# Kernel tuning notes

Hardware: AMD Instinct MI355X
Metric: run time of the kernel (lower is better)

The kernel has to match this reference:

```python
import jax, jax.numpy as jnp
import numpy as np

B, Q, K, DQ, DK, DV, H = 16, 64, 512, 512, 512, 512, 256
MASK_VAL = -1e6


def setup_inputs() -> dict:
    key = jax.random.key(0)
    k1, k2, k3, k4, k5, k6, k7 = jax.random.split(key, 7)
    return {
        "queries": jax.random.normal(k1, (B, Q, DQ), dtype=jnp.float32),
        "keys": jax.random.normal(k2, (B, K, DK), dtype=jnp.float32),
        "values": jax.random.normal(k3, (B, K, DV), dtype=jnp.float32),
        "valid_lens": jax.random.randint(k4, (B,), 1, K + 1, dtype=jnp.int32),
        "Wq": jax.random.normal(k5, (DQ, H), dtype=jnp.float32) * (1.0 / np.sqrt(DQ)),
        "Wk": jax.random.normal(k6, (DK, H), dtype=jnp.float32) * (1.0 / np.sqrt(DK)),
        "Wv": jax.random.normal(k7, (H,), dtype=jnp.float32) * (1.0 / np.sqrt(H)),
    }


def reference(queries, keys, values, valid_lens, Wq, Wk, Wv):
    # Project queries and keys into the shared additive-attention space.
    q = jnp.einsum("bqd,dh->bqh", queries, Wq)   # [B,Q,H]
    k = jnp.einsum("bkd,dh->bkh", keys, Wk)      # [B,K,H]
    # Bahdanau additive scoring: tanh(q + k) projected to a scalar per (q,k).
    feats = jnp.tanh(q[:, :, None, :] + k[:, None, :, :])  # [B,Q,K,H]
    scores = jnp.einsum("bqkh,h->bqk", feats, Wv)           # [B,Q,K]
    # Masked softmax over the key axis (positions >= valid_len masked out).
    mask = jnp.arange(K)[None, None, :] < valid_lens[:, None, None]  # [B,1,K]
    scores = jnp.where(mask, scores, MASK_VAL)
    attn = jax.nn.softmax(scores, axis=-1)                  # [B,Q,K]
    # Dropout is identity in eval mode; weighted sum of values.
    return jnp.einsum("bqk,bkv->bqv", attn, values)         # [B,Q,DV]
```

## Files before the change

kernel.cpp:

```cpp
#include <hip/hip_runtime.h>

#define LOG2E 1.4426950408889634f
#define TWO_LOG2E 2.8853900817779268f

typedef __attribute__((ext_vector_type(8))) short short8;
typedef __attribute__((ext_vector_type(4))) float f32x4;

__device__ __forceinline__ float e2x(float v) {
    return __builtin_amdgcn_exp2f(v * TWO_LOG2E);
}

__device__ __forceinline__ void split2(float x, float y, unsigned& hi, unsigned& lo) {
    unsigned ux = __float_as_uint(x), uy = __float_as_uint(y);
    float hx = __uint_as_float(ux & 0xffff0000u);
    float hy = __uint_as_float(uy & 0xffff0000u);
    unsigned lx = __float_as_uint(x - hx), ly = __float_as_uint(y - hy);
    hi = (ux >> 16) | (uy & 0xffff0000u);
    lo = (lx >> 16) | (ly & 0xffff0000u);
}

__global__ __launch_bounds__(256) void wprep_kernel(const float* __restrict__ Wq,
                                                    const float* __restrict__ Wk,
                                                    ushort* __restrict__ Wq2T,
                                                    ushort* __restrict__ Wk2T) {
    __shared__ float T[64][65];
    const float* W  = blockIdx.z ? Wk : Wq;
    ushort* W2T     = blockIdx.z ? Wk2T : Wq2T;
    const int t  = threadIdx.x;
    const int k0 = blockIdx.x * 64;
    const int n0 = blockIdx.y * 64;
#pragma unroll
    for (int p = 0; p < 4; ++p) {
        int u  = t + p * 256;
        int kk = u >> 4;
        int nf = (u & 15) * 4;
        float4 w = *reinterpret_cast<const float4*>(&W[(size_t)(k0 + kk) * 256 + n0 + nf]);
        T[nf + 0][kk] = w.x; T[nf + 1][kk] = w.y;
        T[nf + 2][kk] = w.z; T[nf + 3][kk] = w.w;
    }
    __syncthreads();
#pragma unroll
    for (int p = 0; p < 4; ++p) {
        int u  = t + p * 256;
        int n  = u >> 4;
        int kf = (u & 15) * 4;
        float a = T[n][kf], b = T[n][kf + 1], c = T[n][kf + 2], d = T[n][kf + 3];
        unsigned h01, l01, h23, l23;
        split2(a, b, h01, l01);
        split2(c, d, h23, l23);
        int kg = k0 + kf;
        ushort* row = W2T + (size_t)(n0 + n) * 1536 + (kg >> 5) * 96 + (kg & 31);
        uint2 hi; hi.x = h01; hi.y = h23;
        uint2 lo; lo.x = l01; lo.y = l23;
        *reinterpret_cast<uint2*>(row)      = hi;
        *reinterpret_cast<uint2*>(row + 32) = hi;
        *reinterpret_cast<uint2*>(row + 64) = lo;
    }
}

__global__ __launch_bounds__(256) void mfma_proj_kernel(const float* __restrict__ queries,
                                                        const float* __restrict__ keys,
                                                        const ushort* __restrict__ Wq2T,
                                                        const ushort* __restrict__ Wk2T,
                                                        float* __restrict__ Eq,
                                                        float* __restrict__ Ekp) {
    __shared__ float smemf[7680];
    ushort* Ah = reinterpret_cast<ushort*>(smemf);
    ushort* Ws = reinterpret_cast<ushort*>(smemf) + 3072;

    const int t    = threadIdx.x;
    const int mt   = blockIdx.x;
    const int Nb   = blockIdx.y * 128;
    const bool isQ = mt < 32;
    const int mloc = (isQ ? mt : mt - 32) * 32;
    const float4* Asrc4 = reinterpret_cast<const float4*>(isQ ? queries : keys)
                        + (size_t)mloc * 128;
    const ushort* W2T = isQ ? Wq2T : Wk2T;

    const int ln15 = t & 15;
    const int q    = (t >> 4) & 3;
    const int w    = t >> 6;
    const int wn   = w * 32;
    const int am   = t >> 3;
    const int ak   = t & 7;

    const char* gB[6];
#pragma unroll
    for (int i = 0; i < 6; ++i) {
        int o   = i * 4096 + t * 16;
        int row = o / 192;
        int rem = o - row * 192;
        gB[i] = reinterpret_cast<const char*>(W2T) + (size_t)(Nb + row) * 3072 + rem;
    }

    f32x4 acc[2][2];
#pragma unroll
    for (int fm = 0; fm < 2; ++fm)
#pragma unroll
        for (int fn = 0; fn < 2; ++fn) acc[fm][fn] = (f32x4)0.0f;

    float4 ra = Asrc4[(size_t)am * 128 + ak];

    for (int c = 0; c < 16; ++c) {
        __syncthreads();
#pragma unroll
        for (int i = 0; i < 6; ++i) {
            __builtin_amdgcn_global_load_lds(
                reinterpret_cast<const unsigned int*>(gB[i]),
                reinterpret_cast<unsigned int*>(
                    reinterpret_cast<char*>(Ah) + 6144 + i * 4096 + (t >> 6) * 1024),
                16, 0, 0);
            gB[i] += 192;
        }
        {
            unsigned h01, l01, h23, l23;
            split2(ra.x, ra.y, h01, l01);
            split2(ra.z, ra.w, h23, l23);
            uint2 hi; hi.x = h01; hi.y = h23;
            uint2 lo; lo.x = l01; lo.y = l23;
            ushort* row = Ah + am * 96 + ak * 4;
            *reinterpret_cast<uint2*>(row)      = hi;
            *reinterpret_cast<uint2*>(row + 32) = lo;
            *reinterpret_cast<uint2*>(row + 64) = hi;
        }
        if (c < 15) ra = Asrc4[(size_t)am * 128 + (c + 1) * 8 + ak];
        __syncthreads();
#pragma unroll
        for (int s = 0; s < 3; ++s) {
            short8 af[2], bf[2];
#pragma unroll
            for (int fm = 0; fm < 2; ++fm)
                af[fm] = *reinterpret_cast<const short8*>(
                    Ah + (fm * 16 + ln15) * 96 + s * 32 + q * 8);
#pragma unroll
            for (int fn = 0; fn < 2; ++fn)
                bf[fn] = *reinterpret_cast<const short8*>(
                    Ws + (wn + fn * 16 + ln15) * 96 + s * 32 + q * 8);
#pragma unroll
            for (int fm = 0; fm < 2; ++fm)
#pragma unroll
                for (int fn = 0; fn < 2; ++fn)
                    acc[fm][fn] = __builtin_amdgcn_mfma_f32_16x16x32_bf16(
                        af[fm], bf[fn], acc[fm][fn], 0, 0, 0);
        }
    }

    if (isQ) {
#pragma unroll
        for (int fm = 0; fm < 2; ++fm)
#pragma unroll
            for (int fn = 0; fn < 2; ++fn)
#pragma unroll
                for (int r = 0; r < 4; ++r) {
                    int row = mloc + fm * 16 + q * 4 + r;
                    int col = Nb + wn + fn * 16 + ln15;
                    Eq[(size_t)row * 256 + col] = e2x(acc[fm][fn][r]);
                }
    } else {
        __syncthreads();
        float (*Cs)[33] = reinterpret_cast<float(*)[33]>(smemf);
#pragma unroll
        for (int fm = 0; fm < 2; ++fm)
#pragma unroll
            for (int fn = 0; fn < 2; ++fn)
#pragma unroll
                for (int r = 0; r < 4; ++r) {
                    int m_l = fm * 16 + q * 4 + r;
                    int n_l = wn + fn * 16 + ln15;
                    Cs[n_l][m_l] = acc[fm][fn][r];
                }
        __syncthreads();
        const int b      = mloc >> 9;
        const int k0h    = (mloc & 511) >> 1;
        const int h2base = Nb >> 1;
        float4* out4 = reinterpret_cast<float4*>(Ekp);
#pragma unroll
        for (int p = 0; p < 4; ++p) {
            int u   = t + p * 256;
            int h2r = u >> 4;
            int kp  = u & 15;
            int kk  = kp * 2;
            float4 o;
            o.x = e2x(Cs[2 * h2r    ][kk    ]);
            o.y = e2x(Cs[2 * h2r + 1][kk    ]);
            o.z = e2x(Cs[2 * h2r    ][kk + 1]);
            o.w = e2x(Cs[2 * h2r + 1][kk + 1]);
            out4[(size_t)b * 32768 + (size_t)(h2base + h2r) * 256 + k0h + kp] = o;
        }
    }
}

__global__ __launch_bounds__(256) void score_softmax_kernel(
        const float* __restrict__ Eq, const float* __restrict__ Ekp,
        const float* __restrict__ Wv, const int* __restrict__ valid_lens,
        float* __restrict__ attn) {
    __shared__ float redmA[4], redmB[4], redlA[4], redlB[4];

    const int t  = threadIdx.x;
    const int bq = blockIdx.x;
    const int b  = bq >> 5;
    const int q0 = (bq & 31) * 2;

    const float* eqA = Eq + (size_t)(b * 64 + q0) * 256;
    const float* eqB = eqA + 256;
    const float4* ek4 = reinterpret_cast<const float4*>(Ekp) + (size_t)b * 32768 + t;

    float accA0 = 0.f, accA1 = 0.f, accB0 = 0.f, accB1 = 0.f;
#pragma unroll 4
    for (int h2 = 0; h2 < 128; ++h2) {
        const float4 ek = ek4[h2 * 256];
        const float w0 = Wv[2 * h2];
        const float w1 = Wv[2 * h2 + 1];
        {
            const float e0 = eqA[2 * h2], e1 = eqA[2 * h2 + 1];
            float a00 = fmaf(e0, ek.x, 1.0f);
            float a10 = fmaf(e1, ek.y, 1.0f);
            float a01 = fmaf(e0, ek.z, 1.0f);
            float a11 = fmaf(e1, ek.w, 1.0f);
            float d0 = a00 * a10, d1 = a01 * a11;
            float n0 = fmaf(w1, a00, w0 * a10);
            float n1 = fmaf(w1, a01, w0 * a11);
            accA0 = fmaf(n0, __builtin_amdgcn_rcpf(d0), accA0);
            accA1 = fmaf(n1, __builtin_amdgcn_rcpf(d1), accA1);
        }
        {
            const float e0 = eqB[2 * h2], e1 = eqB[2 * h2 + 1];
            float a00 = fmaf(e0, ek.x, 1.0f);
            float a10 = fmaf(e1, ek.y, 1.0f);
            float a01 = fmaf(e0, ek.z, 1.0f);
            float a11 = fmaf(e1, ek.w, 1.0f);
            float d0 = a00 * a10, d1 = a01 * a11;
            float n0 = fmaf(w1, a00, w0 * a10);
            float n1 = fmaf(w1, a01, w0 * a11);
            accB0 = fmaf(n0, __builtin_amdgcn_rcpf(d0), accB0);
            accB1 = fmaf(n1, __builtin_amdgcn_rcpf(d1), accB1);
        }
    }
    float sA0 = -2.0f * accA0, sA1 = -2.0f * accA1;
    float sB0 = -2.0f * accB0, sB1 = -2.0f * accB1;
    const int vl = valid_lens[b];
    const int k0 = 2 * t;
    if (k0     >= vl) { sA0 = -1e6f; sB0 = -1e6f; }
    if (k0 + 1 >= vl) { sA1 = -1e6f; sB1 = -1e6f; }

    const int w = t >> 6;
    float mA = fmaxf(sA0, sA1);
    float mB = fmaxf(sB0, sB1);
#pragma unroll
    for (int off = 32; off > 0; off >>= 1) {
        mA = fmaxf(mA, __shfl_xor(mA, off));
        mB = fmaxf(mB, __shfl_xor(mB, off));
    }
    if ((t & 63) == 0) { redmA[w] = mA; redmB[w] = mB; }
    __syncthreads();
    mA = fmaxf(fmaxf(redmA[0], redmA[1]), fmaxf(redmA[2], redmA[3]));
    mB = fmaxf(fmaxf(redmB[0], redmB[1]), fmaxf(redmB[2], redmB[3]));

    float pA0 = __builtin_amdgcn_exp2f((sA0 - mA) * LOG2E);
    float pA1 = __builtin_amdgcn_exp2f((sA1 - mA) * LOG2E);
    float pB0 = __builtin_amdgcn_exp2f((sB0 - mB) * LOG2E);
    float pB1 = __builtin_amdgcn_exp2f((sB1 - mB) * LOG2E);
    float lA = pA0 + pA1, lB = pB0 + pB1;
#pragma unroll
    for (int off = 32; off > 0; off >>= 1) {
        lA += __shfl_xor(lA, off);
        lB += __shfl_xor(lB, off);
    }
    if ((t & 63) == 0) { redlA[w] = lA; redlB[w] = lB; }
    __syncthreads();
    lA = (redlA[0] + redlA[1]) + (redlA[2] + redlA[3]);
    lB = (redlB[0] + redlB[1]) + (redlB[2] + redlB[3]);
    const float invA = 1.0f / lA;
    const float invB = 1.0f / lB;

    float2* attn2 = reinterpret_cast<float2*>(attn);
    float2 oA; oA.x = pA0 * invA; oA.y = pA1 * invA;
    float2 oB; oB.x = pB0 * invB; oB.y = pB1 * invB;
    attn2[(size_t)(b * 64 + q0) * 256 + t]       = oA;
    attn2[(size_t)(b * 64 + q0 + 1) * 256 + t]   = oB;
}

__global__ __launch_bounds__(256) void pv_kernel(const float* __restrict__ attn,
                                                 const float* __restrict__ values,
                                                 float* __restrict__ out) {
    __shared__ __align__(16) float Ps[8][516];
    __shared__ __align__(16) float Vs[2][32][128];

    const int t  = threadIdx.x;
    const int b  = blockIdx.z;
    const int q0 = blockIdx.y * 8;
    const int vt = blockIdx.x;

    const float4* attn4 = reinterpret_cast<const float4*>(attn) + (size_t)(b * 64 + q0) * 128;
#pragma unroll
    for (int p = 0; p < 4; ++p) {
        int u  = t + p * 256;
        int qr = u >> 7;
        int c4 = u & 127;
        *reinterpret_cast<float4*>(&Ps[qr][c4 * 4]) = attn4[(size_t)qr * 128 + c4];
    }

    const char* vbase = reinterpret_cast<const char*>(values)
                      + ((size_t)b * 512 * 512 + (size_t)vt * 128) * 4
                      + (size_t)(t >> 5) * 2048 + (size_t)(t & 31) * 16;
    char* ldsV0 = reinterpret_cast<char*>(&Vs[0][0][0]) + (t >> 6) * 1024;

    const int lane = t & 63;
    const int w    = t >> 6;
    const int v4   = lane & 31;
    const int ksub = lane >> 5;

    float4 acc0 = make_float4(0.f, 0.f, 0.f, 0.f);
    float4 acc1 = make_float4(0.f, 0.f, 0.f, 0.f);

#pragma unroll
    for (int i = 0; i < 4; ++i)
        __builtin_amdgcn_global_load_lds(
            reinterpret_cast<const unsigned int*>(vbase + (size_t)i * 8 * 2048),
            reinterpret_cast<unsigned int*>(ldsV0 + i * 4096), 16, 0, 0);
    __syncthreads();

    for (int c = 0; c < 16; ++c) {
        if (c < 15) {
            char* dst = reinterpret_cast<char*>(&Vs[(c + 1) & 1][0][0]) + (t >> 6) * 1024;
            const char* src = vbase + (size_t)(c + 1) * 65536;
#pragma unroll
            for (int i = 0; i < 4; ++i)
                __builtin_amdgcn_global_load_lds(
                    reinterpret_cast<const unsigned int*>(src + (size_t)i * 8 * 2048),
                    reinterpret_cast<unsigned int*>(dst + i * 4096), 16, 0, 0);
        }

        const float (*V)[128] = Vs[c & 1];
        const float* pr0 = &Ps[2 * w][c * 32];
        const float* pr1 = &Ps[2 * w + 1][c * 32];
#pragma unroll
        for (int kk = 0; kk < 4; ++kk) {
            int kb = kk * 8 + ksub * 4;
            float4 V0 = *reinterpret_cast<const float4*>(&V[kb + 0][v4 * 4]);
            float4 V1 = *reinterpret_cast<const float4*>(&V[kb + 1][v4 * 4]);
            float4 V2 = *reinterpret_cast<const float4*>(&V[kb + 2][v4 * 4]);
            float4 V3 = *reinterpret_cast<const float4*>(&V[kb + 3][v4 * 4]);
            float4 p0 = *reinterpret_cast<const float4*>(&pr0[kb]);
            float4 p1 = *reinterpret_cast<const float4*>(&pr1[kb]);
            acc0.x = fmaf(p0.x, V0.x, acc0.x); acc0.y = fmaf(p0.x, V0.y, acc0.y);
            acc0.z = fmaf(p0.x, V0.z, acc0.z); acc0.w = fmaf(p0.x, V0.w, acc0.w);
            acc0.x = fmaf(p0.y, V1.x, acc0.x); acc0.y = fmaf(p0.y, V1.y, acc0.y);
            acc0.z = fmaf(p0.y, V1.z, acc0.z); acc0.w = fmaf(p0.y, V1.w, acc0.w);
            acc0.x = fmaf(p0.z, V2.x, acc0.x); acc0.y = fmaf(p0.z, V2.y, acc0.y);
            acc0.z = fmaf(p0.z, V2.z, acc0.z); acc0.w = fmaf(p0.z, V2.w, acc0.w);
            acc0.x = fmaf(p0.w, V3.x, acc0.x); acc0.y = fmaf(p0.w, V3.y, acc0.y);
            acc0.z = fmaf(p0.w, V3.z, acc0.z); acc0.w = fmaf(p0.w, V3.w, acc0.w);
            acc1.x = fmaf(p1.x, V0.x, acc1.x); acc1.y = fmaf(p1.x, V0.y, acc1.y);
            acc1.z = fmaf(p1.x, V0.z, acc1.z); acc1.w = fmaf(p1.x, V0.w, acc1.w);
            acc1.x = fmaf(p1.y, V1.x, acc1.x); acc1.y = fmaf(p1.y, V1.y, acc1.y);
            acc1.z = fmaf(p1.y, V1.z, acc1.z); acc1.w = fmaf(p1.y, V1.w, acc1.w);
            acc1.x = fmaf(p1.z, V2.x, acc1.x); acc1.y = fmaf(p1.z, V2.y, acc1.y);
            acc1.z = fmaf(p1.z, V2.z, acc1.z); acc1.w = fmaf(p1.z, V2.w, acc1.w);
            acc1.x = fmaf(p1.w, V3.x, acc1.x); acc1.y = fmaf(p1.w, V3.y, acc1.y);
            acc1.z = fmaf(p1.w, V3.z, acc1.z); acc1.w = fmaf(p1.w, V3.w, acc1.w);
        }
        __syncthreads();
    }

    acc0.x += __shfl_xor(acc0.x, 32); acc0.y += __shfl_xor(acc0.y, 32);
    acc0.z += __shfl_xor(acc0.z, 32); acc0.w += __shfl_xor(acc0.w, 32);
    acc1.x += __shfl_xor(acc1.x, 32); acc1.y += __shfl_xor(acc1.y, 32);
    acc1.z += __shfl_xor(acc1.z, 32); acc1.w += __shfl_xor(acc1.w, 32);
    if (ksub == 0) {
        float4* out4 = reinterpret_cast<float4*>(out);
        out4[(size_t)(b * 64 + q0 + 2 * w) * 128 + vt * 32 + v4]     = acc0;
        out4[(size_t)(b * 64 + q0 + 2 * w + 1) * 128 + vt * 32 + v4] = acc1;
    }
}

extern "C" void kernel_launch(void* const* d_in, const int* in_sizes, int n_in,
                              void* d_out, int out_size, void* d_ws, size_t ws_size,
                              hipStream_t stream) {
    (void)in_sizes; (void)n_in; (void)out_size; (void)ws_size;
    const float* queries    = (const float*)d_in[0];
    const float* keys       = (const float*)d_in[1];
    const float* values     = (const float*)d_in[2];
    const int*   valid_lens = (const int*)d_in[3];
    const float* Wq         = (const float*)d_in[4];
    const float* Wk         = (const float*)d_in[5];
    const float* Wv         = (const float*)d_in[6];
    float* out = (float*)d_out;

    float* ws    = (float*)d_ws;
    float* Eq    = ws;
    float* Ekp   = ws + 262144;
    float* attn  = ws + 262144 + 2097152;
    ushort* Wq2T = (ushort*)(ws + 2883584);
    ushort* Wk2T = Wq2T + 393216;

    hipLaunchKernelGGL(wprep_kernel, dim3(8, 4, 2), dim3(256), 0, stream,
                       Wq, Wk, Wq2T, Wk2T);
    hipLaunchKernelGGL(mfma_proj_kernel, dim3(288, 2), dim3(256), 0, stream,
                       queries, keys, Wq2T, Wk2T, Eq, Ekp);
    hipLaunchKernelGGL(score_softmax_kernel, dim3(512), dim3(256), 0, stream,
                       Eq, Ekp, Wv, valid_lens, attn);
    hipLaunchKernelGGL(pv_kernel, dim3(4, 8, 16), dim3(256), 0, stream, attn, values, out);
}
```

Measured before the change: 141.6 us.

## Retile score kernel over 8 queries and move softmax into PV kernel

The score kernel now processes 8 queries by 128 keys per block, staging Eq and Wv in shared memory and splitting the H dimension across two thread halves, so each Ek load is reused across 8 queries instead of 2. It writes raw masked scores. The softmax max, exp and normalisation move into the PV kernel, which computes them on the score rows already staged in LDS, removing block-wide reductions from the score kernel. The cost is redundant softmax work, since each of the 4 value-tile blocks recomputes the softmax for the same rows, plus an extra LDS partial-sum pass in the score kernel.

```diff
diff --git a/kernel.cpp b/kernel.cpp
--- a/kernel.cpp
+++ b/kernel.cpp
@@ -190,97 +190,64 @@
     }
 }
 
-__global__ __launch_bounds__(256) void score_softmax_kernel(
+__global__ __launch_bounds__(256) void score_raw_kernel(
         const float* __restrict__ Eq, const float* __restrict__ Ekp,
         const float* __restrict__ Wv, const int* __restrict__ valid_lens,
-        float* __restrict__ attn) {
-    __shared__ float redmA[4], redmB[4], redlA[4], redlB[4];
-
+        float* __restrict__ scores) {
+    __shared__ float Eqs[8][256];
+    __shared__ float Wvs[256];
+    __shared__ float Sh[2][8][128];
     const int t  = threadIdx.x;
-    const int bq = blockIdx.x;
-    const int b  = bq >> 5;
-    const int q0 = (bq & 31) * 2;
-
-    const float* eqA = Eq + (size_t)(b * 64 + q0) * 256;
-    const float* eqB = eqA + 256;
-    const float4* ek4 = reinterpret_cast<const float4*>(Ekp) + (size_t)b * 32768 + t;
-
-    float accA0 = 0.f, accA1 = 0.f, accB0 = 0.f, accB1 = 0.f;
+    const int kb = blockIdx.x * 128;
+    const int q0 = blockIdx.y * 8;
+    const int b  = blockIdx.z;
+
+    const float4* eq4 = reinterpret_cast<const float4*>(Eq + (size_t)(b * 64 + q0) * 256);
+#pragma unroll
+    for (int i = 0; i < 2; ++i) {
+        int u = t + i * 256;
+        *reinterpret_cast<float4*>(&Eqs[u >> 6][(u & 63) * 4]) = eq4[u];
+    }
+    Wvs[t] = Wv[t];
+    __syncthreads();
+
+    const int kl = t & 127;
+    const int hh = t >> 7;
+    const float2* ek2 = reinterpret_cast<const float2*>(Ekp)
+                      + (size_t)b * 65536 + (size_t)hh * 32768 + kb + kl;
+
+    float acc[8] = {0.f, 0.f, 0.f, 0.f, 0.f, 0.f, 0.f, 0.f};
 #pragma unroll 4
-    for (int h2 = 0; h2 < 128; ++h2) {
-        const float4 ek = ek4[h2 * 256];
-        const float w0 = Wv[2 * h2];
-        const float w1 = Wv[2 * h2 + 1];
-        {
-            const float e0 = eqA[2 * h2], e1 = eqA[2 * h2 + 1];
-            float a00 = fmaf(e0, ek.x, 1.0f);
-            float a10 = fmaf(e1, ek.y, 1.0f);
-            float a01 = fmaf(e0, ek.z, 1.0f);
-            float a11 = fmaf(e1, ek.w, 1.0f);
-            float d0 = a00 * a10, d1 = a01 * a11;
-            float n0 = fmaf(w1, a00, w0 * a10);
-            float n1 = fmaf(w1, a01, w0 * a11);
-            accA0 = fmaf(n0, __builtin_amdgcn_rcpf(d0), accA0);
-            accA1 = fmaf(n1, __builtin_amdgcn_rcpf(d1), accA1);
-        }
-        {
-            const float e0 = eqB[2 * h2], e1 = eqB[2 * h2 + 1];
-            float a00 = fmaf(e0, ek.x, 1.0f);
-            float a10 = fmaf(e1, ek.y, 1.0f);
-            float a01 = fmaf(e0, ek.z, 1.0f);
-            float a11 = fmaf(e1, ek.w, 1.0f);
-            float d0 = a00 * a10, d1 = a01 * a11;
-            float n0 = fmaf(w1, a00, w0 * a10);
-            float n1 = fmaf(w1, a01, w0 * a11);
-            accB0 = fmaf(n0, __builtin_amdgcn_rcpf(d0), accB0);
-            accB1 = fmaf(n1, __builtin_amdgcn_rcpf(d1), accB1);
-        }
-    }
-    float sA0 = -2.0f * accA0, sA1 = -2.0f * accA1;
-    float sB0 = -2.0f * accB0, sB1 = -2.0f * accB1;
+    for (int i = 0; i < 64; ++i) {
+        float2 ek = ek2[(size_t)i * 512];
+        int h2 = hh * 64 + i;
+        float w0 = Wvs[2 * h2], w1 = Wvs[2 * h2 + 1];
+#pragma unroll
+        for (int q = 0; q < 8; ++q) {
+            float e0 = Eqs[q][2 * h2], e1 = Eqs[q][2 * h2 + 1];
+            float a0 = fmaf(e0, ek.x, 1.0f);
+            float a1 = fmaf(e1, ek.y, 1.0f);
+            float d  = a0 * a1;
+            float n  = fmaf(w1, a0, w0 * a1);
+            acc[q] = fmaf(n, __builtin_amdgcn_rcpf(d), acc[q]);
+        }
+    }
+#pragma unroll
+    for (int q = 0; q < 8; ++q) Sh[hh][q][kl] = acc[q];
+    __syncthreads();
+
     const int vl = valid_lens[b];
-    const int k0 = 2 * t;
-    if (k0     >= vl) { sA0 = -1e6f; sB0 = -1e6f; }
-    if (k0 + 1 >= vl) { sA1 = -1e6f; sB1 = -1e6f; }
-
-    const int w = t >> 6;
-    float mA = fmaxf(sA0, sA1);
-    float mB = fmaxf(sB0, sB1);
-#pragma unroll
-    for (int off = 32; off > 0; off >>= 1) {
-        mA = fmaxf(mA, __shfl_xor(mA, off));
-        mB = fmaxf(mB, __shfl_xor(mB, off));
-    }
-    if ((t & 63) == 0) { redmA[w] = mA; redmB[w] = mB; }
-    __syncthreads();
-    mA = fmaxf(fmaxf(redmA[0], redmA[1]), fmaxf(redmA[2], redmA[3]));
-    mB = fmaxf(fmaxf(redmB[0], redmB[1]), fmaxf(redmB[2], redmB[3]));
-
-    float pA0 = __builtin_amdgcn_exp2f((sA0 - mA) * LOG2E);
-    float pA1 = __builtin_amdgcn_exp2f((sA1 - mA) * LOG2E);
-    float pB0 = __builtin_amdgcn_exp2f((sB0 - mB) * LOG2E);
-    float pB1 = __builtin_amdgcn_exp2f((sB1 - mB) * LOG2E);
-    float lA = pA0 + pA1, lB = pB0 + pB1;
-#pragma unroll
-    for (int off = 32; off > 0; off >>= 1) {
-        lA += __shfl_xor(lA, off);
-        lB += __shfl_xor(lB, off);
-    }
-    if ((t & 63) == 0) { redlA[w] = lA; redlB[w] = lB; }
-    __syncthreads();
-    lA = (redlA[0] + redlA[1]) + (redlA[2] + redlA[3]);
-    lB = (redlB[0] + redlB[1]) + (redlB[2] + redlB[3]);
-    const float invA = 1.0f / lA;
-    const float invB = 1.0f / lB;
-
-    float2* attn2 = reinterpret_cast<float2*>(attn);
-    float2 oA; oA.x = pA0 * invA; oA.y = pA1 * invA;
-    float2 oB; oB.x = pB0 * invB; oB.y = pB1 * invB;
-    attn2[(size_t)(b * 64 + q0) * 256 + t]       = oA;
-    attn2[(size_t)(b * 64 + q0 + 1) * 256 + t]   = oB;
-}
-
-__global__ __launch_bounds__(256) void pv_kernel(const float* __restrict__ attn,
+#pragma unroll
+    for (int i = 0; i < 4; ++i) {
+        int u = t + i * 256;
+        int q = u >> 7, k = u & 127;
+        float s = -2.0f * (Sh[0][q][k] + Sh[1][q][k]);
+        if (kb + k >= vl) s = -1e6f;
+        scores[(size_t)(b * 64 + q0 + q) * 512 + kb + k] = s;
+    }
+}
+
+__global__ __launch_bounds__(256) void pv_kernel(const float* __restrict__ scores,
                                                  const float* __restrict__ values,
                                                  float* __restrict__ out) {
     __shared__ __align__(16) float Ps[8][516];
@@ -291,13 +258,13 @@
     const int q0 = blockIdx.y * 8;
     const int vt = blockIdx.x;
 
-    const float4* attn4 = reinterpret_cast<const float4*>(attn) + (size_t)(b * 64 + q0) * 128;
+    const float4* sc4 = reinterpret_cast<const float4*>(scores) + (size_t)(b * 64 + q0) * 128;
 #pragma unroll
     for (int p = 0; p < 4; ++p) {
         int u  = t + p * 256;
         int qr = u >> 7;
         int c4 = u & 127;
-        *reinterpret_cast<float4*>(&Ps[qr][c4 * 4]) = attn4[(size_t)qr * 128 + c4];
+        *reinterpret_cast<float4*>(&Ps[qr][c4 * 4]) = sc4[(size_t)qr * 128 + c4];
     }
 
     const char* vbase = reinterpret_cast<const char*>(values)
@@ -309,9 +276,6 @@
     const int w    = t >> 6;
     const int v4   = lane & 31;
     const int ksub = lane >> 5;
-
-    float4 acc0 = make_float4(0.f, 0.f, 0.f, 0.f);
-    float4 acc1 = make_float4(0.f, 0.f, 0.f, 0.f);
 
 #pragma unroll
     for (int i = 0; i < 4; ++i)
@@ -319,6 +283,31 @@
             reinterpret_cast<const unsigned int*>(vbase + (size_t)i * 8 * 2048),
             reinterpret_cast<unsigned int*>(ldsV0 + i * 4096), 16, 0, 0);
     __syncthreads();
+
+#pragma unroll
+    for (int rr = 0; rr < 2; ++rr) {
+        const int r = 2 * w + rr;
+        float v[8];
+        float m = -1e30f;
+#pragma unroll
+        for (int i = 0; i < 8; ++i) { v[i] = Ps[r][lane + i * 64]; m = fmaxf(m, v[i]); }
+#pragma unroll
+        for (int off = 32; off > 0; off >>= 1) m = fmaxf(m, __shfl_xor(m, off));
+        float s = 0.f;
+#pragma unroll
+        for (int i = 0; i < 8; ++i) {
+            v[i] = __builtin_amdgcn_exp2f((v[i] - m) * LOG2E);
+            s += v[i];
+        }
+#pragma unroll
+        for (int off = 32; off > 0; off >>= 1) s += __shfl_xor(s, off);
+        float inv = 1.0f / s;
+#pragma unroll
+        for (int i = 0; i < 8; ++i) Ps[r][lane + i * 64] = v[i] * inv;
+    }
+
+    float4 acc0 = make_float4(0.f, 0.f, 0.f, 0.f);
+    float4 acc1 = make_float4(0.f, 0.f, 0.f, 0.f);
 
     for (int c = 0; c < 16; ++c) {
         if (c < 15) {
@@ -387,18 +376,19 @@
     const float* Wv         = (const float*)d_in[6];
     float* out = (float*)d_out;
 
-    float* ws    = (float*)d_ws;
-    float* Eq    = ws;
-    float* Ekp   = ws + 262144;
-    float* attn  = ws + 262144 + 2097152;
-    ushort* Wq2T = (ushort*)(ws + 2883584);
-    ushort* Wk2T = Wq2T + 393216;
+    float* ws     = (float*)d_ws;
+    float* Eq     = ws;
+    float* Ekp    = ws + 262144;
+    float* scores = ws + 262144 + 2097152;
+    ushort* Wq2T  = (ushort*)(ws + 2883584);
+    ushort* Wk2T  = Wq2T + 393216;
 
     hipLaunchKernelGGL(wprep_kernel, dim3(8, 4, 2), dim3(256), 0, stream,
                        Wq, Wk, Wq2T, Wk2T);
     hipLaunchKernelGGL(mfma_proj_kernel, dim3(288, 2), dim3(256), 0, stream,
                        queries, keys, Wq2T, Wk2T, Eq, Ekp);
-    hipLaunchKernelGGL(score_softmax_kernel, dim3(512), dim3(256), 0, stream,
-                       Eq, Ekp, Wv, valid_lens, attn);
-    hipLaunchKernelGGL(pv_kernel, dim3(4, 8, 16), dim3(256), 0, stream, attn, values, out);
-}
+    hipLaunchKernelGGL(score_raw_kernel, dim3(4, 8, 16), dim3(256), 0, stream,
+                       Eq, Ekp, Wv, valid_lens, scores);
+    hipLaunchKernelGGL(pv_kernel, dim3(4, 8, 16), dim3(256), 0, stream,
+                       scores, values, out);
+}
```

After: 143.2 us. About the same (+1.1%).
